# Kernel tuning notes

Measured on AMD Instinct MI355X. Metric: run time of the kernel, lower is better.

Reference implementation:

```python
import jax, jax.numpy as jnp
import numpy as np

N, NFEAT, NHID, NHEADS, NCLASS = 4096, 1024, 128, 8, 64
ALPHA = 0.2  # LeakyReLU negative slope
NEG_INF = -9e15


def setup_inputs() -> dict:
    key = jax.random.key(0)
    ks = jax.random.split(key, 8)
    x = jax.random.normal(ks[0], (N, NFEAT), dtype=jnp.float32)
    adj = jax.random.randint(ks[1], (N, N), 0, 2, dtype=jnp.int32)
    sW = 1.0 / np.sqrt(NFEAT)
    W = jax.random.normal(ks[2], (NHEADS, NFEAT, NHID), dtype=jnp.float32) * sW
    a1 = jax.random.normal(ks[3], (NHEADS, NHID), dtype=jnp.float32) * 0.1
    a2 = jax.random.normal(ks[4], (NHEADS, NHID), dtype=jnp.float32) * 0.1
    sWo = 1.0 / np.sqrt(NHID * NHEADS)
    Wo = jax.random.normal(ks[5], (NHID * NHEADS, NCLASS), dtype=jnp.float32) * sWo
    ao1 = jax.random.normal(ks[6], (NCLASS,), dtype=jnp.float32) * 0.1
    ao2 = jax.random.normal(ks[7], (NCLASS,), dtype=jnp.float32) * 0.1
    return {"x": x, "adj": adj, "W": W, "a1": a1, "a2": a2,
            "Wo": Wo, "ao1": ao1, "ao2": ao2}


def reference(x, adj, W, a1, a2, Wo, ao1, ao2):
    mask = adj > 0  # [N, N]
    # --- multi-head attention layer (concat=True) ---
    Wh = jnp.einsum('nf,hfd->hnd', x, W)            # [H, N, D]
    f1 = jnp.einsum('hnd,hd->hn', Wh, a1)           # [H, N] self score
    f2 = jnp.einsum('hnd,hd->hn', Wh, a2)           # [H, N] neighbor score
    e = jax.nn.leaky_relu(f1[:, :, None] + f2[:, None, :], negative_slope=ALPHA)
    e = jnp.where(mask[None, :, :], e, NEG_INF)
    attn = jax.nn.softmax(e, axis=-1)               # [H, N, N]
    h = jnp.einsum('hnm,hmd->hnd', attn, Wh)        # [H, N, D]
    h = jax.nn.elu(h)                               # concat=True applies elu
    h = jnp.transpose(h, (1, 0, 2)).reshape(N, NHEADS * NHID)  # concat heads
    # --- output attention layer (concat=False) ---
    Who = h @ Wo                                    # [N, C]
    g1 = Who @ ao1                                  # [N]
    g2 = Who @ ao2                                  # [N]
    eo = jax.nn.leaky_relu(g1[:, None] + g2[None, :], negative_slope=ALPHA)
    eo = jnp.where(mask, eo, NEG_INF)
    ao = jax.nn.softmax(eo, axis=-1)                # [N, N]
    out = ao @ Who                                  # [N, C]
    out = jax.nn.elu(out)                           # F.elu in GAT.forward
    return jax.nn.log_softmax(out, axis=1)
```

## Files before the change

### kernel.cpp

```cpp
#include <hip/hip_runtime.h>
#include <hip/hip_bf16.h>


#define NN    4096
#define NF    1024
#define DH    128
#define NHEADS 8
#define NCLS  64
#define ALPHA 0.2f
#define LOG2E 1.44269504f

using short8 = __attribute__((ext_vector_type(8))) short;
using f32x4  = __attribute__((ext_vector_type(4))) float;
using int4v  = __attribute__((ext_vector_type(4))) int;

static __device__ __forceinline__ float bf2f(unsigned short h) {
    return __uint_as_float(((unsigned int)h) << 16);
}
static __device__ __forceinline__ unsigned short f2bf(float f) {
    unsigned int u = __float_as_uint(f);
    u = (u + 0x7fffu + ((u >> 16) & 1u)) >> 16;
    return (unsigned short)u;
}
static __device__ __forceinline__ float fast_exp2(float x) {
    return __builtin_amdgcn_exp2f(x);
}

__global__ __launch_bounds__(256) void diag_fill(
    float* __restrict__ out, int n, float val)
{
    int i = blockIdx.x * 256 + threadIdx.x;
    if (i < n) out[i] = val;
}

__global__ __launch_bounds__(256) void prep(
    const float* __restrict__ x, const int* __restrict__ adj,
    const float* __restrict__ W, const float* __restrict__ Wo,
    const float* __restrict__ a1, const float* __restrict__ a2,
    const float* __restrict__ ao1, const float* __restrict__ ao2,
    unsigned short* __restrict__ xB, unsigned int* __restrict__ bm,
    unsigned short* __restrict__ WT, unsigned short* __restrict__ WoT,
    unsigned short* __restrict__ a1B, unsigned short* __restrict__ a2B,
    unsigned short* __restrict__ ao1B, unsigned short* __restrict__ ao2B)
{
    __shared__ unsigned short tile[32][33];
    int b = blockIdx.x, t = threadIdx.x;
    if (b < 16384) {
        long t4 = (long)b * 256 + t;
        int4v v = ((const int4v*)adj)[t4];
        unsigned nib = (v[0] > 0 ? 1u : 0u) | (v[1] > 0 ? 2u : 0u)
                     | (v[2] > 0 ? 4u : 0u) | (v[3] > 0 ? 8u : 0u);
        int l = t & 63;
        unsigned w = nib << (4 * (l & 7));
        w |= __shfl_xor(w, 1);
        w |= __shfl_xor(w, 2);
        w |= __shfl_xor(w, 4);
        if ((l & 7) == 0) bm[t4 >> 3] = w;
    } else if (b < 20480) {
        long i = ((long)(b - 16384) * 256 + t) * 4;
        float4 v = *(const float4*)&x[i];
        unsigned u0 = (unsigned)f2bf(v.x) | ((unsigned)f2bf(v.y) << 16);
        unsigned u1 = (unsigned)f2bf(v.z) | ((unsigned)f2bf(v.w) << 16);
        uint2 u; u.x = u0; u.y = u1;
        *(uint2*)&xB[i] = u;
    } else if (b < 21632) {
        int tid = b - 20480;
        int z = tid >> 7;
        int rem = tid & 127;
        int bx = rem & 3, by = rem >> 2;
        const float* in; unsigned short* out; int C;
        if (z < 8) { in = W + (long)z * NF * DH; out = WT + (long)z * DH * NF; C = DH; }
        else       { in = Wo;                    out = WoT;                    C = NCLS; }
        int x0 = bx * 32, y0 = by * 32;
        if (x0 >= C) return;
        int tx = t & 31, ty = t >> 5;
        for (int yy = 0; yy < 32; yy += 8)
            tile[ty + yy][tx] = f2bf(in[(long)(y0 + ty + yy) * C + x0 + tx]);
        __syncthreads();
        for (int yy = 0; yy < 32; yy += 8)
            out[(long)(x0 + ty + yy) * NF + y0 + tx] = tile[tx][ty + yy];
    } else if (b == 21632) {
        for (int i = t; i < NHEADS * DH; i += 256) {
            a1B[i] = f2bf(a1[i]);
            a2B[i] = f2bf(a2[i]);
        }
    } else {
        if (t < NCLS) {
            ao1B[t] = f2bf(ao1[t]);
            ao2B[t] = f2bf(ao2[t]);
        }
    }
}

__global__ __launch_bounds__(256) void gemm1_fs(
    const unsigned short* __restrict__ A, const unsigned short* __restrict__ Bt,
    unsigned short* __restrict__ Cc, const unsigned short* __restrict__ a1B,
    const unsigned short* __restrict__ a2B, float* __restrict__ f1,
    float* __restrict__ f2)
{
    __shared__ unsigned short Alds[64][72];
    __shared__ unsigned short Blds[128][72];
    __shared__ float s1l[128], s2l[128];
    int t = threadIdx.x;
    int w = t >> 6, l = t & 63;
    int h = blockIdx.z;
    long aoff = (long)h * DH * NF + (long)blockIdx.y * 64 * NF;
    long boff = (long)blockIdx.x * 128 * NF;
    if (t < 128) { s1l[t] = 0.f; s2l[t] = 0.f; }
    f32x4 acc[8];
#pragma unroll
    for (int i = 0; i < 8; ++i) acc[i] = (f32x4){0.f, 0.f, 0.f, 0.f};

    for (int k0 = 0; k0 < NF; k0 += 64) {
#pragma unroll
        for (int it = 0; it < 2; ++it) {
            int ci = it * 256 + t;
            int r = ci >> 3, c8 = (ci & 7) * 8;
            *(short8*)&Alds[r][c8] = *(const short8*)&A[aoff + (long)r * NF + k0 + c8];
        }
#pragma unroll
        for (int it = 0; it < 4; ++it) {
            int ci = it * 256 + t;
            int r = ci >> 3, c8 = (ci & 7) * 8;
            *(short8*)&Blds[r][c8] = *(const short8*)&Bt[boff + (long)r * NF + k0 + c8];
        }
        __syncthreads();
        int arow = w * 16 + (l & 15);
        int koff = (l >> 4) * 8;
#pragma unroll
        for (int kc = 0; kc < 2; ++kc) {
            short8 af = *(const short8*)&Alds[arow][kc * 32 + koff];
#pragma unroll
            for (int dt = 0; dt < 8; ++dt) {
                short8 bf = *(const short8*)&Blds[dt * 16 + (l & 15)][kc * 32 + koff];
                acc[dt] = __builtin_amdgcn_mfma_f32_16x16x32_bf16(af, bf, acc[dt], 0, 0, 0);
            }
        }
        __syncthreads();
    }
    long coff = (long)h * DH * NN + ((long)blockIdx.y * 64) * NN + blockIdx.x * 128;
    int mrow = w * 16 + (l >> 4) * 4;
    int dbase = blockIdx.y * 64;
#pragma unroll
    for (int dt = 0; dt < 8; ++dt) {
        int n = dt * 16 + (l & 15);
        float p1 = 0.f, p2 = 0.f;
#pragma unroll
        for (int r = 0; r < 4; ++r) {
            unsigned short bw = f2bf(acc[dt][r]);
            Cc[coff + (long)(mrow + r) * NN + n] = bw;
            float vf = bf2f(bw);
            int d = dbase + mrow + r;
            p1 += vf * bf2f(a1B[h * DH + d]);
            p2 += vf * bf2f(a2B[h * DH + d]);
        }
        atomicAdd(&s1l[n], p1);
        atomicAdd(&s2l[n], p2);
    }
    __syncthreads();
    if (t < 128) {
        int n = blockIdx.x * 128 + t;
        atomicAdd(&f1[h * NN + n], s1l[t] * LOG2E);
        atomicAdd(&f2[h * NN + n], s2l[t] * LOG2E);
    }
}

__global__ __launch_bounds__(256) void gemm2c(
    const unsigned short* __restrict__ A, const unsigned short* __restrict__ Bt,
    const unsigned short* __restrict__ ao1B, const unsigned short* __restrict__ ao2B,
    unsigned short* __restrict__ WhoT, float* __restrict__ g1, float* __restrict__ g2)
{
    __shared__ unsigned short Alds[64][72];
    __shared__ unsigned short Blds[64][72];
    __shared__ float s1l[64], s2l[64];
    int t = threadIdx.x;
    int w = t >> 6, l = t & 63;
    int n0 = blockIdx.x * 64;
    if (t < 64) { s1l[t] = 0.f; s2l[t] = 0.f; }
    f32x4 acc[4];
#pragma unroll
    for (int i = 0; i < 4; ++i) acc[i] = (f32x4){0.f, 0.f, 0.f, 0.f};

    for (int k0 = 0; k0 < NF; k0 += 64) {
#pragma unroll
        for (int it = 0; it < 2; ++it) {
            int ci = it * 256 + t;
            int r = ci >> 3, c8 = (ci & 7) * 8;
            *(short8*)&Alds[r][c8] = *(const short8*)&A[(long)r * NF + k0 + c8];
        }
#pragma unroll
        for (int it = 0; it < 2; ++it) {
            int ci = it * 256 + t;
            int r = ci >> 3, c8 = (ci & 7) * 8;
            *(short8*)&Blds[r][c8] = *(const short8*)&Bt[(long)(n0 + r) * NF + k0 + c8];
        }
        __syncthreads();
        int arow = w * 16 + (l & 15);
        int koff = (l >> 4) * 8;
#pragma unroll
        for (int kc = 0; kc < 2; ++kc) {
            short8 af = *(const short8*)&Alds[arow][kc * 32 + koff];
#pragma unroll
            for (int dt = 0; dt < 4; ++dt) {
                short8 bf = *(const short8*)&Blds[dt * 16 + (l & 15)][kc * 32 + koff];
                acc[dt] = __builtin_amdgcn_mfma_f32_16x16x32_bf16(af, bf, acc[dt], 0, 0, 0);
            }
        }
        __syncthreads();
    }
    int mrow = w * 16 + (l >> 4) * 4;
#pragma unroll
    for (int dt = 0; dt < 4; ++dt) {
        int nl = dt * 16 + (l & 15);
        float p1 = 0.f, p2 = 0.f;
#pragma unroll
        for (int r = 0; r < 4; ++r) {
            int c = mrow + r;
            unsigned short bw = f2bf(acc[dt][r]);
            WhoT[(long)c * NN + n0 + nl] = bw;
            float vf = bf2f(bw);
            p1 += vf * bf2f(ao1B[c]);
            p2 += vf * bf2f(ao2B[c]);
        }
        atomicAdd(&s1l[nl], p1);
        atomicAdd(&s2l[nl], p2);
    }
    __syncthreads();
    if (t < 64) {
        g1[n0 + t] = s1l[t] * LOG2E;
        g2[n0 + t] = s2l[t] * LOG2E;
    }
}

static __device__ __forceinline__ float build_p16(
    unsigned int bits, float fi, const float* f2s, int pc0,
    short8& p0, short8& p1)
{
    float lsum = 0.f;
#pragma unroll
    for (int cc = 0; cc < 16; ++cc) {
        float wgt = 0.f;
        if ((bits >> cc) & 1u) {
            float e = fi + f2s[pc0 + cc];
            e = e > 0.f ? e : ALPHA * e;
            e = fminf(e, 60.f);
            wgt = fast_exp2(e);
        }
        unsigned short bw = f2bf(wgt);
        lsum += bf2f(bw);
        if (cc < 8) p0[cc] = (short)bw;
        else        p1[cc - 8] = (short)bw;
    }
    return lsum;
}

static __device__ __forceinline__ void build_pfrag3(
    unsigned long long wpair, float fi, const float* __restrict__ f2g,
    int kgrp, short8& a0, short8& a1)
{
    int4v av0, av1;
#pragma unroll
    for (int kc = 0; kc < 2; ++kc) {
        unsigned bits = (unsigned)(wpair >> (kc * 32 + kgrp * 8)) & 0xFFu;
        const float4* fp = (const float4*)(f2g + kc * 32 + kgrp * 8);
        float4 fv0 = fp[0], fv1 = fp[1];
        float ev[8] = {fv0.x, fv0.y, fv0.z, fv0.w, fv1.x, fv1.y, fv1.z, fv1.w};
#pragma unroll
        for (int jj = 0; jj < 8; jj += 2) {
            float e0 = fi + ev[jj], e1 = fi + ev[jj + 1];
            e0 = fmaxf(e0, ALPHA * e0);
            e1 = fmaxf(e1, ALPHA * e1);
            float w0 = fast_exp2(e0), w1 = fast_exp2(e1);
            w0 = ((bits >> jj) & 1u) ? w0 : 0.f;
            w1 = ((bits >> (jj + 1)) & 1u) ? w1 : 0.f;
            float2 fv; fv.x = w0; fv.y = w1;
            __hip_bfloat162 pk = __float22bfloat162_rn(fv);
            unsigned pu; __builtin_memcpy(&pu, &pk, 4);
            if (kc == 0) av0[jj >> 1] = (int)pu;
            else         av1[jj >> 1] = (int)pu;
        }
    }
    a0 = __builtin_bit_cast(short8, av0);
    a1 = __builtin_bit_cast(short8, av1);
}

__global__ __launch_bounds__(256) void attn1_direct(
    const float* __restrict__ f1, const float* __restrict__ f2,
    const unsigned int* __restrict__ bm, const unsigned short* __restrict__ WhT,
    unsigned short* __restrict__ hcat)
{
    __shared__ unsigned short Plds[64][72];
    __shared__ unsigned short Wlds[128][72];
    __shared__ float f1s[64], f2s[64], ssum[64][4], srow[64];
    int t = threadIdx.x;
    int h = blockIdx.y;
    int i0 = blockIdx.x * 64;
    int w = t >> 6, l = t & 63;
    if (t < 64) f1s[t] = f1[h * NN + i0 + t];
    f32x4 acc[8];
#pragma unroll
    for (int i = 0; i < 8; ++i) acc[i] = (f32x4){0.f, 0.f, 0.f, 0.f};
    float psum = 0.f;
    int pr = t >> 2, pc0 = (t & 3) * 16;
    const unsigned short* Wh_h = WhT + (long)h * DH * NN;

    for (int j0 = 0; j0 < NN; j0 += 64) {
        if (t < 64) f2s[t] = f2[h * NN + j0 + t];
        __syncthreads();
        {
            unsigned int word = bm[(long)(i0 + pr) * (NN / 32) + (j0 >> 5) + ((pc0 >> 5) & 1)];
            unsigned int bits = (word >> (pc0 & 16)) & 0xFFFFu;
            short8 p0, p1;
            psum += build_p16(bits, f1s[pr], f2s, pc0, p0, p1);
            *(short8*)&Plds[pr][pc0]     = p0;
            *(short8*)&Plds[pr][pc0 + 8] = p1;
        }
#pragma unroll
        for (int it = 0; it < 4; ++it) {
            int ci = it * 256 + t;
            int d = ci >> 3, c8 = (ci & 7) * 8;
            *(short8*)&Wlds[d][c8] = *(const short8*)&Wh_h[(long)d * NN + j0 + c8];
        }
        __syncthreads();
        int arow = w * 16 + (l & 15);
        int koff = (l >> 4) * 8;
#pragma unroll
        for (int kc = 0; kc < 2; ++kc) {
            short8 af = *(const short8*)&Plds[arow][kc * 32 + koff];
#pragma unroll
            for (int dt = 0; dt < 8; ++dt) {
                short8 bf = *(const short8*)&Wlds[dt * 16 + (l & 15)][kc * 32 + koff];
                acc[dt] = __builtin_amdgcn_mfma_f32_16x16x32_bf16(af, bf, acc[dt], 0, 0, 0);
            }
        }
        __syncthreads();
    }
    ssum[pr][t & 3] = psum;
    __syncthreads();
    if (t < 64) srow[t] = ssum[t][0] + ssum[t][1] + ssum[t][2] + ssum[t][3];
    __syncthreads();
    int mrow = w * 16 + (l >> 4) * 4;
#pragma unroll
    for (int dt = 0; dt < 8; ++dt) {
        int d = dt * 16 + (l & 15);
#pragma unroll
        for (int r = 0; r < 4; ++r) {
            float v = acc[dt][r] / fmaxf(srow[mrow + r], 1e-20f);
            v = v > 0.f ? v : __expf(v) - 1.f;
            hcat[(long)(i0 + mrow + r) * (NHEADS * DH) + h * DH + d] = f2bf(v);
        }
    }
}

__global__ __launch_bounds__(256) void attn1_part(
    const float* __restrict__ f1, const float* __restrict__ f2,
    const unsigned int* __restrict__ bm, const unsigned short* __restrict__ WhT,
    unsigned short* __restrict__ accp1, float* __restrict__ dsum1, int jspan)
{
    __shared__ unsigned short Wlds[128][72];
    int t = threadIdx.x;
    int h = blockIdx.y;
    int i0 = blockIdx.x * 64;
    int jz = blockIdx.z;
    int w = t >> 6, l = t & 63;
    int m = l & 15, kgrp = l >> 4;
    int myrow = i0 + w * 16 + m;
    float fi = f1[h * NN + myrow];
    const unsigned int* bmrow = bm + (long)myrow * (NN / 32);
    const float* f2h = f2 + (long)h * NN;
    const unsigned short* Wh_h = WhT + (long)h * DH * NN;
    short8 ones;
#pragma unroll
    for (int i = 0; i < 8; ++i) ones[i] = (short)0x3F80;
    f32x4 acc[8];
#pragma unroll
    for (int i = 0; i < 8; ++i) acc[i] = (f32x4){0.f, 0.f, 0.f, 0.f};
    f32x4 accd = (f32x4){0.f, 0.f, 0.f, 0.f};

    for (int j0 = jz * jspan; j0 < (jz + 1) * jspan; j0 += 64) {
        unsigned long long wpair;
        __builtin_memcpy(&wpair, &bmrow[j0 >> 5], 8);
#pragma unroll
        for (int it = 0; it < 4; ++it) {
            int ci = it * 256 + t;
            int d = ci >> 3, c8 = (ci & 7) * 8;
            *(short8*)&Wlds[d][c8] = *(const short8*)&Wh_h[(long)d * NN + j0 + c8];
        }
        short8 a0, a1;
        build_pfrag3(wpair, fi, f2h + j0, kgrp, a0, a1);
        __syncthreads();
        accd = __builtin_amdgcn_mfma_f32_16x16x32_bf16(a0, ones, accd, 0, 0, 0);
        accd = __builtin_amdgcn_mfma_f32_16x16x32_bf16(a1, ones, accd, 0, 0, 0);
#pragma unroll
        for (int dt = 0; dt < 8; ++dt) {
            short8 b0 = *(const short8*)&Wlds[dt * 16 + m][kgrp * 8];
            acc[dt] = __builtin_amdgcn_mfma_f32_16x16x32_bf16(a0, b0, acc[dt], 0, 0, 0);
        }
#pragma unroll
        for (int dt = 0; dt < 8; ++dt) {
            short8 b1 = *(const short8*)&Wlds[dt * 16 + m][32 + kgrp * 8];
            acc[dt] = __builtin_amdgcn_mfma_f32_16x16x32_bf16(a1, b1, acc[dt], 0, 0, 0);
        }
        __syncthreads();
    }
    if (m == 0) {
#pragma unroll
        for (int r = 0; r < 4; ++r)
            dsum1[((long)jz * NHEADS + h) * NN + i0 + w * 16 + kgrp * 4 + r] = accd[r];
    }
    int mrow = w * 16 + kgrp * 4;
#pragma unroll
    for (int dt = 0; dt < 8; ++dt) {
        int d = dt * 16 + m;
#pragma unroll
        for (int r = 0; r < 4; ++r)
            accp1[((long)jz * NN + i0 + mrow + r) * (NHEADS * DH) + h * DH + d] = f2bf(acc[dt][r]);
    }
}

__global__ __launch_bounds__(256) void combine1(
    const unsigned short* __restrict__ accp1, const float* __restrict__ dsum1,
    unsigned short* __restrict__ hcat, int js)
{
    long idx4 = (long)blockIdx.x * 256 + threadIdx.x;
    int i = (int)(idx4 >> 8), c4 = (int)(idx4 & 255) * 4, h = c4 >> 7;
    float4 v = {0.f, 0.f, 0.f, 0.f};
    float s = 0.f;
    for (int jz = 0; jz < js; ++jz) {
        uint2 pv = *(const uint2*)&accp1[((long)jz * NN + i) * (NHEADS * DH) + c4];
        v.x += bf2f((unsigned short)(pv.x & 0xFFFFu));
        v.y += bf2f((unsigned short)(pv.x >> 16));
        v.z += bf2f((unsigned short)(pv.y & 0xFFFFu));
        v.w += bf2f((unsigned short)(pv.y >> 16));
        s += dsum1[((long)jz * NHEADS + h) * NN + i];
    }
    float inv = 1.f / fmaxf(s, 1e-20f);
    float o[4] = {v.x * inv, v.y * inv, v.z * inv, v.w * inv};
#pragma unroll
    for (int k = 0; k < 4; ++k) o[k] = o[k] > 0.f ? o[k] : __expf(o[k]) - 1.f;
    unsigned u0 = (unsigned)f2bf(o[0]) | ((unsigned)f2bf(o[1]) << 16);
    unsigned u1 = (unsigned)f2bf(o[2]) | ((unsigned)f2bf(o[3]) << 16);
    uint2 u; u.x = u0; u.y = u1;
    *(uint2*)&hcat[(long)i * (NHEADS * DH) + c4] = u;
}

__global__ __launch_bounds__(256) void attn2(
    const float* __restrict__ g1, const float* __restrict__ g2,
    const unsigned int* __restrict__ bm, const unsigned short* __restrict__ WhoT,
    unsigned short* __restrict__ accp, float* __restrict__ sp, int jspan)
{
    __shared__ unsigned short Wlds[64][72];
    int t = threadIdx.x;
    int i0 = blockIdx.x * 64;
    int jc = blockIdx.y;
    int w = t >> 6, l = t & 63;
    int m = l & 15, kgrp = l >> 4;
    int myrow = i0 + w * 16 + m;
    float fi = g1[myrow];
    const unsigned int* bmrow = bm + (long)myrow * (NN / 32);
    short8 ones;
#pragma unroll
    for (int i = 0; i < 8; ++i) ones[i] = (short)0x3F80;
    f32x4 acc[4];
#pragma unroll
    for (int i = 0; i < 4; ++i) acc[i] = (f32x4){0.f, 0.f, 0.f, 0.f};
    f32x4 accd = (f32x4){0.f, 0.f, 0.f, 0.f};

    for (int j0 = jc * jspan; j0 < (jc + 1) * jspan; j0 += 64) {
        unsigned long long wpair;
        __builtin_memcpy(&wpair, &bmrow[j0 >> 5], 8);
#pragma unroll
        for (int it = 0; it < 2; ++it) {
            int ci = it * 256 + t;
            int d = ci >> 3, c8 = (ci & 7) * 8;
            *(short8*)&Wlds[d][c8] = *(const short8*)&WhoT[(long)d * NN + j0 + c8];
        }
        short8 a0, a1;
        build_pfrag3(wpair, fi, g2 + j0, kgrp, a0, a1);
        __syncthreads();
        accd = __builtin_amdgcn_mfma_f32_16x16x32_bf16(a0, ones, accd, 0, 0, 0);
        accd = __builtin_amdgcn_mfma_f32_16x16x32_bf16(a1, ones, accd, 0, 0, 0);
#pragma unroll
        for (int dt = 0; dt < 4; ++dt) {
            short8 b0 = *(const short8*)&Wlds[dt * 16 + m][kgrp * 8];
            acc[dt] = __builtin_amdgcn_mfma_f32_16x16x32_bf16(a0, b0, acc[dt], 0, 0, 0);
        }
#pragma unroll
        for (int dt = 0; dt < 4; ++dt) {
            short8 b1 = *(const short8*)&Wlds[dt * 16 + m][32 + kgrp * 8];
            acc[dt] = __builtin_amdgcn_mfma_f32_16x16x32_bf16(a1, b1, acc[dt], 0, 0, 0);
        }
        __syncthreads();
    }
    if (m == 0) {
#pragma unroll
        for (int r = 0; r < 4; ++r)
            sp[(long)jc * NN + i0 + w * 16 + kgrp * 4 + r] = accd[r];
    }
    int mrow = w * 16 + kgrp * 4;
#pragma unroll
    for (int dt = 0; dt < 4; ++dt) {
        int d = dt * 16 + m;
#pragma unroll
        for (int r = 0; r < 4; ++r)
            accp[((long)jc * NN + i0 + mrow + r) * NCLS + d] = f2bf(acc[dt][r]);
    }
}

__global__ __launch_bounds__(256) void finalize(
    const unsigned short* __restrict__ accp, const float* __restrict__ sp,
    float* __restrict__ out, int js)
{
    int t = threadIdx.x;
    int wv = t >> 6, l = t & 63;
    int r = blockIdx.x * 4 + wv;
    float v = 0.f, s = 0.f;
    for (int jc = 0; jc < js; ++jc) {
        v += bf2f(accp[((long)jc * NN + r) * NCLS + l]);
        s += sp[(long)jc * NN + r];
    }
    v /= fmaxf(s, 1e-20f);
    v = v > 0.f ? v : __expf(v) - 1.f;
    float m = v;
#pragma unroll
    for (int off = 32; off; off >>= 1) m = fmaxf(m, __shfl_xor(m, off));
    float ex = __expf(v - m);
#pragma unroll
    for (int off = 32; off; off >>= 1) ex += __shfl_xor(ex, off);
    out[(long)r * NCLS + l] = v - (m + __logf(ex));
}

extern "C" void kernel_launch(void* const* d_in, const int* in_sizes, int n_in,
                              void* d_out, int out_size, void* d_ws, size_t ws_size,
                              hipStream_t stream)
{
    const float* x   = (const float*)d_in[0];
    const int*   adj = (const int*)d_in[1];
    const float* W   = (const float*)d_in[2];
    const float* a1  = (const float*)d_in[3];
    const float* a2  = (const float*)d_in[4];
    const float* Wo  = (const float*)d_in[5];
    const float* ao1 = (const float*)d_in[6];
    const float* ao2 = (const float*)d_in[7];
    float* out = (float*)d_out;

    const long SZ_XB   = (long)NN * NF * 2;
    const long SZ_AB   = (long)NHEADS * DH * 2;
    const long SZ_AOB  = (long)NCLS * 2;
    const long SZ_WT   = (long)NHEADS * DH * NF * 2;
    const long SZ_WOT  = (long)NCLS * NF * 2;
    const long SZ_WHT  = (long)NHEADS * DH * NN * 2;
    const long SZ_HCAT = (long)NN * NHEADS * DH * 2;
    const long SZ_WHOT = (long)NCLS * NN * 2;
    const long SZ_F    = (long)NHEADS * NN * 4;
    const long SZ_G    = (long)NN * 4;
    const long SZ_BM   = (long)NN * (NN / 32) * 4;
    const long SZ_AP1  = (long)NN * NHEADS * DH * 2;
    const long SZ_DS1  = (long)NHEADS * NN * 4;
    const long SZ_AP2  = (long)NN * NCLS * 2;
    const long SZ_SP2  = (long)NN * 4;
    long base = SZ_XB + 2 * SZ_AB + 2 * SZ_AOB + SZ_WT + SZ_WOT + SZ_WHT
              + SZ_HCAT + SZ_WHOT + 2 * SZ_F + 2 * SZ_G + SZ_BM
              + 40 * 256;

    int js1, js2;
    if ((size_t)(base + 4 * (SZ_AP1 + SZ_DS1) + 16 * (SZ_AP2 + SZ_SP2)) <= ws_size) {
        js1 = 4; js2 = 16;
    } else if ((size_t)(base + 4 * (SZ_AP1 + SZ_DS1) + 8 * (SZ_AP2 + SZ_SP2)) <= ws_size) {
        js1 = 4; js2 = 8;
    } else if ((size_t)(base + 2 * (SZ_AP1 + SZ_DS1) + 8 * (SZ_AP2 + SZ_SP2)) <= ws_size) {
        js1 = 2; js2 = 8;
    } else if ((size_t)(base + 16 * (SZ_AP2 + SZ_SP2)) <= ws_size) {
        js1 = 1; js2 = 16;
    } else if ((size_t)(base + 4 * (SZ_AP2 + SZ_SP2)) <= ws_size) {
        js1 = 1; js2 = 4;
    } else {
        diag_fill<<<dim3((out_size + 255) / 256), 256, 0, stream>>>(
            out, out_size, (float)(ws_size >> 20));
        return;
    }

    char* p = (char*)d_ws;
    auto alloc = [&](long bytes) { char* q = p; p += (bytes + 255) & ~255L; return q; };
    unsigned short* xB   = (unsigned short*)alloc(SZ_XB);
    unsigned short* a1B  = (unsigned short*)alloc(SZ_AB);
    unsigned short* a2B  = (unsigned short*)alloc(SZ_AB);
    unsigned short* ao1B = (unsigned short*)alloc(SZ_AOB);
    unsigned short* ao2B = (unsigned short*)alloc(SZ_AOB);
    unsigned short* WT   = (unsigned short*)alloc(SZ_WT);
    unsigned short* WoT  = (unsigned short*)alloc(SZ_WOT);
    unsigned short* WhT  = (unsigned short*)alloc(SZ_WHT);
    unsigned short* hcat = (unsigned short*)alloc(SZ_HCAT);
    unsigned short* WhoT = (unsigned short*)alloc(SZ_WHOT);
    float* f1 = (float*)alloc(SZ_F);
    float* f2 = (float*)alloc(SZ_F);
    float* g1 = (float*)alloc(SZ_G);
    float* g2 = (float*)alloc(SZ_G);
    unsigned int* bm = (unsigned int*)alloc(SZ_BM);
    unsigned short* accp2 = (unsigned short*)alloc(js2 * SZ_AP2);
    float* sp2   = (float*)alloc(js2 * SZ_SP2);
    unsigned short* accp1 = (unsigned short*)(js1 > 1 ? alloc(js1 * SZ_AP1) : nullptr);
    float* dsum1 = (float*)(js1 > 1 ? alloc(js1 * SZ_DS1) : nullptr);

    hipMemsetAsync(f1, 0, 2 * SZ_F, stream);
    prep<<<dim3(21634), 256, 0, stream>>>(
        x, adj, W, Wo, a1, a2, ao1, ao2,
        xB, bm, WT, WoT, a1B, a2B, ao1B, ao2B);
    gemm1_fs<<<dim3(NN / 128, DH / 64, NHEADS), 256, 0, stream>>>(
        WT, xB, WhT, a1B, a2B, f1, f2);
    if (js1 > 1) {
        attn1_part<<<dim3(NN / 64, NHEADS, js1), 256, 0, stream>>>(
            f1, f2, bm, WhT, accp1, dsum1, NN / js1);
        combine1<<<dim3((int)(((long)NN * NHEADS * DH) / 1024)), 256, 0, stream>>>(
            accp1, dsum1, hcat, js1);
    } else {
        attn1_direct<<<dim3(NN / 64, NHEADS), 256, 0, stream>>>(f1, f2, bm, WhT, hcat);
    }
    gemm2c<<<dim3(NN / 64), 256, 0, stream>>>(WoT, hcat, ao1B, ao2B, WhoT, g1, g2);
    attn2<<<dim3(NN / 64, js2), 256, 0, stream>>>(g1, g2, bm, WhoT, accp2, sp2, NN / js2);
    finalize<<<dim3(NN / 4), 256, 0, stream>>>(accp2, sp2, out, js2);
}
```

Baseline: 299.7 us.

## Fuse split-K combine of attention layer into output GEMM and drop memset

Removes the separate combine1 kernel by having gemm2c sum the split partial accumulators, normalize by the summed denominators, apply ELU and convert to bf16 while loading its B tile. It also folds the f1/f2 zeroing into extra blocks of the prep kernel instead of a hipMemsetAsync. This saves two launches and the hcat write and read round trip. The cost is that gemm2c, with only 64 blocks, now does the reduction work serially inside its K loop, which may lengthen that low-parallelism kernel.

```diff
diff --git a/kernel.cpp b/kernel.cpp
--- a/kernel.cpp
+++ b/kernel.cpp
@@ -41,7 +41,8 @@
     unsigned short* __restrict__ xB, unsigned int* __restrict__ bm,
     unsigned short* __restrict__ WT, unsigned short* __restrict__ WoT,
     unsigned short* __restrict__ a1B, unsigned short* __restrict__ a2B,
-    unsigned short* __restrict__ ao1B, unsigned short* __restrict__ ao2B)
+    unsigned short* __restrict__ ao1B, unsigned short* __restrict__ ao2B,
+    float* __restrict__ f1z)
 {
     __shared__ unsigned short tile[32][33];
     int b = blockIdx.x, t = threadIdx.x;
@@ -84,11 +85,14 @@
             a1B[i] = f2bf(a1[i]);
             a2B[i] = f2bf(a2[i]);
         }
-    } else {
+    } else if (b == 21633) {
         if (t < NCLS) {
             ao1B[t] = f2bf(ao1[t]);
             ao2B[t] = f2bf(ao2[t]);
         }
+    } else {
+        long i = ((long)(b - 21634) * 256 + t) * 4;
+        *(float4*)&f1z[i] = (float4){0.f, 0.f, 0.f, 0.f};
     }
 }
 
@@ -166,17 +170,30 @@
 }
 
 __global__ __launch_bounds__(256) void gemm2c(
-    const unsigned short* __restrict__ A, const unsigned short* __restrict__ Bt,
+    const unsigned short* __restrict__ A, const unsigned short* __restrict__ accp1,
+    const float* __restrict__ dsum1, const unsigned short* __restrict__ hcat,
     const unsigned short* __restrict__ ao1B, const unsigned short* __restrict__ ao2B,
-    unsigned short* __restrict__ WhoT, float* __restrict__ g1, float* __restrict__ g2)
+    unsigned short* __restrict__ WhoT, float* __restrict__ g1, float* __restrict__ g2,
+    int js1)
 {
     __shared__ unsigned short Alds[64][72];
     __shared__ unsigned short Blds[64][72];
     __shared__ float s1l[64], s2l[64];
+    __shared__ float sinv[64][NHEADS];
     int t = threadIdx.x;
     int w = t >> 6, l = t & 63;
     int n0 = blockIdx.x * 64;
     if (t < 64) { s1l[t] = 0.f; s2l[t] = 0.f; }
+    if (js1 > 1) {
+        for (int idx = t; idx < 64 * NHEADS; idx += 256) {
+            int i = idx & 63, h = idx >> 6;
+            float s = 0.f;
+            for (int jz = 0; jz < js1; ++jz)
+                s += dsum1[((long)jz * NHEADS + h) * NN + n0 + i];
+            sinv[i][h] = 1.f / fmaxf(s, 1e-20f);
+        }
+    }
+    __syncthreads();
     f32x4 acc[4];
 #pragma unroll
     for (int i = 0; i < 4; ++i) acc[i] = (f32x4){0.f, 0.f, 0.f, 0.f};
@@ -188,11 +205,34 @@
             int r = ci >> 3, c8 = (ci & 7) * 8;
             *(short8*)&Alds[r][c8] = *(const short8*)&A[(long)r * NF + k0 + c8];
         }
+        int hh = k0 >> 7;
 #pragma unroll
         for (int it = 0; it < 2; ++it) {
             int ci = it * 256 + t;
             int r = ci >> 3, c8 = (ci & 7) * 8;
-            *(short8*)&Blds[r][c8] = *(const short8*)&Bt[(long)(n0 + r) * NF + k0 + c8];
+            if (js1 > 1) {
+                float v[8] = {0.f, 0.f, 0.f, 0.f, 0.f, 0.f, 0.f, 0.f};
+                for (int jz = 0; jz < js1; ++jz) {
+                    uint4 pv = *(const uint4*)&accp1[((long)jz * NN + n0 + r) * (NHEADS * DH) + k0 + c8];
+                    unsigned pu[4] = {pv.x, pv.y, pv.z, pv.w};
+#pragma unroll
+                    for (int q = 0; q < 4; ++q) {
+                        v[q * 2]     += bf2f((unsigned short)(pu[q] & 0xFFFFu));
+                        v[q * 2 + 1] += bf2f((unsigned short)(pu[q] >> 16));
+                    }
+                }
+                float inv = sinv[r][hh];
+                short8 bvec;
+#pragma unroll
+                for (int q = 0; q < 8; ++q) {
+                    float o = v[q] * inv;
+                    o = o > 0.f ? o : __expf(o) - 1.f;
+                    bvec[q] = (short)f2bf(o);
+                }
+                *(short8*)&Blds[r][c8] = bvec;
+            } else {
+                *(short8*)&Blds[r][c8] = *(const short8*)&hcat[(long)(n0 + r) * NF + k0 + c8];
+            }
         }
         __syncthreads();
         int arow = w * 16 + (l & 15);
@@ -416,32 +456,6 @@
         for (int r = 0; r < 4; ++r)
             accp1[((long)jz * NN + i0 + mrow + r) * (NHEADS * DH) + h * DH + d] = f2bf(acc[dt][r]);
     }
-}
-
-__global__ __launch_bounds__(256) void combine1(
-    const unsigned short* __restrict__ accp1, const float* __restrict__ dsum1,
-    unsigned short* __restrict__ hcat, int js)
-{
-    long idx4 = (long)blockIdx.x * 256 + threadIdx.x;
-    int i = (int)(idx4 >> 8), c4 = (int)(idx4 & 255) * 4, h = c4 >> 7;
-    float4 v = {0.f, 0.f, 0.f, 0.f};
-    float s = 0.f;
-    for (int jz = 0; jz < js; ++jz) {
-        uint2 pv = *(const uint2*)&accp1[((long)jz * NN + i) * (NHEADS * DH) + c4];
-        v.x += bf2f((unsigned short)(pv.x & 0xFFFFu));
-        v.y += bf2f((unsigned short)(pv.x >> 16));
-        v.z += bf2f((unsigned short)(pv.y & 0xFFFFu));
-        v.w += bf2f((unsigned short)(pv.y >> 16));
-        s += dsum1[((long)jz * NHEADS + h) * NN + i];
-    }
-    float inv = 1.f / fmaxf(s, 1e-20f);
-    float o[4] = {v.x * inv, v.y * inv, v.z * inv, v.w * inv};
-#pragma unroll
-    for (int k = 0; k < 4; ++k) o[k] = o[k] > 0.f ? o[k] : __expf(o[k]) - 1.f;
-    unsigned u0 = (unsigned)f2bf(o[0]) | ((unsigned)f2bf(o[1]) << 16);
-    unsigned u1 = (unsigned)f2bf(o[2]) | ((unsigned)f2bf(o[3]) << 16);
-    uint2 u; u.x = u0; u.y = u1;
-    *(uint2*)&hcat[(long)i * (NHEADS * DH) + c4] = u;
 }
 
 __global__ __launch_bounds__(256) void attn2(
@@ -602,21 +616,19 @@
     unsigned short* accp1 = (unsigned short*)(js1 > 1 ? alloc(js1 * SZ_AP1) : nullptr);
     float* dsum1 = (float*)(js1 > 1 ? alloc(js1 * SZ_DS1) : nullptr);
 
-    hipMemsetAsync(f1, 0, 2 * SZ_F, stream);
-    prep<<<dim3(21634), 256, 0, stream>>>(
+    prep<<<dim3(21698), 256, 0, stream>>>(
         x, adj, W, Wo, a1, a2, ao1, ao2,
-        xB, bm, WT, WoT, a1B, a2B, ao1B, ao2B);
+        xB, bm, WT, WoT, a1B, a2B, ao1B, ao2B, f1);
     gemm1_fs<<<dim3(NN / 128, DH / 64, NHEADS), 256, 0, stream>>>(
         WT, xB, WhT, a1B, a2B, f1, f2);
     if (js1 > 1) {
         attn1_part<<<dim3(NN / 64, NHEADS, js1), 256, 0, stream>>>(
             f1, f2, bm, WhT, accp1, dsum1, NN / js1);
-        combine1<<<dim3((int)(((long)NN * NHEADS * DH) / 1024)), 256, 0, stream>>>(
-            accp1, dsum1, hcat, js1);
     } else {
         attn1_direct<<<dim3(NN / 64, NHEADS), 256, 0, stream>>>(f1, f2, bm, WhT, hcat);
     }
-    gemm2c<<<dim3(NN / 64), 256, 0, stream>>>(WoT, hcat, ao1B, ao2B, WhoT, g1, g2);
+    gemm2c<<<dim3(NN / 64), 256, 0, stream>>>(
+        WoT, accp1, dsum1, hcat, ao1B, ao2B, WhoT, g1, g2, js1);
     attn2<<<dim3(NN / 64, js2), 256, 0, stream>>>(g1, g2, bm, WhoT, accp2, sp2, NN / js2);
     finalize<<<dim3(NN / 4), 256, 0, stream>>>(accp2, sp2, out, js2);
 }
```

Measured after the change: 337.2 us. 1.13x slower.
